# Kernel optimization log

Hardware: AMD Instinct MI355X
Metric: run time of the kernel (lower is better)

Reference implementation:

```python
import jax, jax.numpy as jnp
import numpy as np

N_NODES = 100000
N_EDGES = 1600000
D_IN = 128
D_OUT = 128
NEG_SLOPE = 0.01  # torch F.leaky_relu default


def setup_inputs() -> dict:
    key = jax.random.key(0)
    k1, k2, k3, k4, k5 = jax.random.split(key, 5)
    h = jax.random.normal(k1, (N_NODES, D_IN), dtype=jnp.float32)
    # nn.Linear default init scale ~ 1/sqrt(fan_in)
    W = jax.random.normal(k2, (D_IN, D_OUT), dtype=jnp.float32) / np.sqrt(D_IN)
    attn_w = jax.random.normal(k3, (2 * D_OUT,), dtype=jnp.float32) / np.sqrt(2 * D_OUT)
    edge_src = jax.random.randint(k4, (N_EDGES,), 0, N_NODES, dtype=jnp.int32)
    edge_dst = jax.random.randint(k5, (N_EDGES,), 0, N_NODES, dtype=jnp.int32)
    return {"h": h, "W": W, "attn_w": attn_w, "edge_src": edge_src, "edge_dst": edge_dst}


def reference(h, W, attn_w, edge_src, edge_dst):
    n = h.shape[0]
    d = W.shape[1]
    z = h @ W                                   # [N, d]
    # attention_func(cat([z_src, z_dst])) == z_src @ a[:d] + z_dst @ a[d:]
    s_src = z @ attn_w[:d]                      # [N]
    s_dst = z @ attn_w[d:]                      # [N]
    e = jax.nn.leaky_relu(s_src[edge_src] + s_dst[edge_dst], NEG_SLOPE)  # [E]
    # segment softmax over incoming edges of each dst node
    m = jax.ops.segment_max(e, edge_dst, num_segments=n)   # [N], -inf for empty
    ex = jnp.exp(e - m[edge_dst])                           # [E]
    denom = jax.ops.segment_sum(ex, edge_dst, num_segments=n)  # [N]
    alpha = ex / denom[edge_dst]                             # [E]
    # weighted neighbor sum: sum_j alpha_ij * z_j
    out = jax.ops.segment_sum(alpha[:, None] * z[edge_src], edge_dst, num_segments=n)
    return out
```

## Files before the change

kernel.cpp:

```cpp
#include <hip/hip_runtime.h>

#define D 128
#define NEG_SLOPE 0.01f
#define BSHIFT 7
#define B1 1024
#define STR 136
#define SCHUNK 3072
#define SEPT 6
#define SLOT 2560

typedef __attribute__((ext_vector_type(8))) short short8;
typedef __attribute__((ext_vector_type(4))) float floatx4;

__device__ __forceinline__ unsigned f2bf_rne(float x) {
    unsigned u = __float_as_uint(x);
    return (u + 0x7fffu + ((u >> 16) & 1u)) >> 16;
}
#define BF_LO(u) __uint_as_float((u) << 16)
#define BF_HI(u) __uint_as_float((u) & 0xffff0000u)

__global__ void init_gcur(int* __restrict__ gcur) {
    const int i = threadIdx.x;
    gcur[i] = i * SLOT;
}

__global__ __launch_bounds__(512) void sort_scatter(const int* __restrict__ esrc,
                                                    const int* __restrict__ edst,
                                                    int* __restrict__ gcur,
                                                    int* __restrict__ pairs, int E) {
    __shared__ int cnt[B1], exc[B1], gbs[B1], cur[B1];
    __shared__ int spk[SCHUNK];
    __shared__ unsigned short sbkt[SCHUNK];
    __shared__ int wtot[8];
    const int t = threadIdx.x;
    cnt[t] = 0; cnt[t + 512] = 0; cur[t] = 0; cur[t + 512] = 0;
    __syncthreads();

    const int e0 = blockIdx.x * SCHUNK;
    const int n  = min(SCHUNK, E - e0);

    int pk[SEPT], bk[SEPT];
#pragma unroll
    for (int k = 0; k < SEPT; ++k) {
        const int i = t + k * 512;
        if (i < n) {
            const int d = edst[e0 + i];
            const int s = esrc[e0 + i];
            bk[k] = d >> BSHIFT;
            pk[k] = (s << BSHIFT) | (d & 127);
            atomicAdd(&cnt[bk[k]], 1);
        } else {
            bk[k] = -1;
        }
    }
    __syncthreads();

    const int c0 = cnt[2 * t], c1 = cnt[2 * t + 1];
    const int s2 = c0 + c1;
    int incl = s2;
#pragma unroll
    for (int o = 1; o < 64; o <<= 1) {
        int v = __shfl_up(incl, o, 64);
        if ((t & 63) >= o) incl += v;
    }
    const int wv = t >> 6;
    if ((t & 63) == 63) wtot[wv] = incl;
    __syncthreads();
    int wpre = 0;
#pragma unroll
    for (int i = 0; i < 8; ++i) wpre += (i < wv) ? wtot[i] : 0;
    const int ex0 = wpre + incl - s2;
    exc[2 * t]     = ex0;
    exc[2 * t + 1] = ex0 + c0;
    if (c0 > 0) gbs[2 * t]     = atomicAdd(&gcur[2 * t], c0);
    if (c1 > 0) gbs[2 * t + 1] = atomicAdd(&gcur[2 * t + 1], c1);
    __syncthreads();

#pragma unroll
    for (int k = 0; k < SEPT; ++k) {
        if (bk[k] >= 0) {
            const int p = exc[bk[k]] + atomicAdd(&cur[bk[k]], 1);
            spk[p]  = pk[k];
            sbkt[p] = (unsigned short)bk[k];
        }
    }
    __syncthreads();

    for (int i = t; i < n; i += 512) {
        const int b = sbkt[i];
        const int pos = gbs[b] + (i - exc[b]);
        if (pos < (b + 1) * SLOT) pairs[pos] = spk[i];
    }
}

__global__ __launch_bounds__(256) void fine_build(const int* __restrict__ pairs,
                                                  const int* __restrict__ gcur,
                                                  int* __restrict__ beg,
                                                  int* __restrict__ ncnt,
                                                  int* __restrict__ adj, int N) {
    __shared__ int cnt[128], sc[128], cur[128];
    const int b = blockIdx.x;
    const int base = b << BSHIFT;
    const int nd = min(128, N - base);
    const int t = threadIdx.x;
    const int s0 = b * SLOT;
    const int e1 = min(gcur[b], s0 + SLOT);
    if (t < 128) { cnt[t] = 0; cur[t] = 0; }
    __syncthreads();
    int pk[10];
#pragma unroll
    for (int k = 0; k < 10; ++k) {
        const int i = s0 + t + k * 256;
        pk[k] = (i < e1) ? pairs[i] : -1;
        if (pk[k] >= 0) atomicAdd(&cnt[pk[k] & 127], 1);
    }
    __syncthreads();
    if (t < 128) sc[t] = cnt[t];
    __syncthreads();
    for (int off = 1; off < 128; off <<= 1) {
        int v = (t < 128 && t >= off) ? sc[t - off] : 0;
        __syncthreads();
        if (t < 128) sc[t] += v;
        __syncthreads();
    }
    if (t < nd) {
        beg[base + t]  = s0 + sc[t] - cnt[t];
        ncnt[base + t] = cnt[t];
    }
    __syncthreads();
#pragma unroll
    for (int k = 0; k < 10; ++k) {
        if (pk[k] >= 0) {
            const int d = pk[k] & 127;
            const int pos = s0 + (sc[d] - cnt[d]) + atomicAdd(&cur[d], 1);
            adj[pos] = pk[k] >> BSHIFT;
        }
    }
}

__global__ __launch_bounds__(256) void gemm_zs(const float* __restrict__ h,
                                               const float* __restrict__ W,
                                               const float* __restrict__ aw,
                                               unsigned short* __restrict__ z,
                                               float* __restrict__ s_src,
                                               float* __restrict__ s_dst, int N) {
    __shared__ unsigned short ws_hi[D * STR];
    __shared__ unsigned short ws_lo[D * STR];
    const int t = threadIdx.x;
    for (int i = t; i < D * D; i += 256) {
        int k = i >> 7, n = i & 127;
        float x = W[i];
        unsigned hi = f2bf_rne(x);
        float hf = __uint_as_float(hi << 16);
        unsigned lo = __float_as_uint(x - hf) >> 16;
        ws_hi[n * STR + k] = (unsigned short)hi;
        ws_lo[n * STR + k] = (unsigned short)lo;
    }
    __syncthreads();

    const int lane = t & 63, quad = lane >> 4, l16 = lane & 15;
    const int rowbase = blockIdx.x * 64 + (t >> 6) * 16;
    const int arow = min(rowbase + l16, N - 1);
    const float* __restrict__ hrow = h + (size_t)arow * D;

    floatx4 acc[8];
#pragma unroll
    for (int ct = 0; ct < 8; ++ct) acc[ct] = (floatx4){0.f, 0.f, 0.f, 0.f};

#pragma unroll
    for (int kk = 0; kk < 4; ++kk) {
        const int k0 = kk * 32 + quad * 8;
        float4 x0 = *(const float4*)&hrow[k0];
        float4 x1 = *(const float4*)&hrow[k0 + 4];
        float xs[8] = {x0.x, x0.y, x0.z, x0.w, x1.x, x1.y, x1.z, x1.w};
        union { short8 v; unsigned short u[8]; } ahi, alo;
#pragma unroll
        for (int i = 0; i < 8; ++i) {
            unsigned hi = f2bf_rne(xs[i]);
            float hf = __uint_as_float(hi << 16);
            ahi.u[i] = (unsigned short)hi;
            alo.u[i] = (unsigned short)(__float_as_uint(xs[i] - hf) >> 16);
        }
#pragma unroll
        for (int ct = 0; ct < 8; ++ct) {
            const int bo = (ct * 16 + l16) * STR + k0;
            short8 bhi = *(const short8*)&ws_hi[bo];
            short8 blo = *(const short8*)&ws_lo[bo];
            acc[ct] = __builtin_amdgcn_mfma_f32_16x16x32_bf16(ahi.v, bhi, acc[ct], 0, 0, 0);
            acc[ct] = __builtin_amdgcn_mfma_f32_16x16x32_bf16(alo.v, bhi, acc[ct], 0, 0, 0);
            acc[ct] = __builtin_amdgcn_mfma_f32_16x16x32_bf16(ahi.v, blo, acc[ct], 0, 0, 0);
        }
    }

#pragma unroll
    for (int ct = 0; ct < 8; ++ct)
#pragma unroll
        for (int reg = 0; reg < 4; ++reg) {
            int r = rowbase + quad * 4 + reg;
            if (r < N)
                z[(size_t)r * D + ct * 16 + l16] = (unsigned short)f2bf_rne(acc[ct][reg]);
        }

    float ps[4] = {0.f, 0.f, 0.f, 0.f}, pd[4] = {0.f, 0.f, 0.f, 0.f};
#pragma unroll
    for (int ct = 0; ct < 8; ++ct) {
        float as = aw[ct * 16 + l16];
        float ad = aw[128 + ct * 16 + l16];
#pragma unroll
        for (int reg = 0; reg < 4; ++reg) {
            ps[reg] = fmaf(acc[ct][reg], as, ps[reg]);
            pd[reg] = fmaf(acc[ct][reg], ad, pd[reg]);
        }
    }
#pragma unroll
    for (int reg = 0; reg < 4; ++reg)
#pragma unroll
        for (int o = 1; o < 16; o <<= 1) {
            ps[reg] += __shfl_xor(ps[reg], o, 64);
            pd[reg] += __shfl_xor(pd[reg], o, 64);
        }
    if (l16 == 0) {
#pragma unroll
        for (int reg = 0; reg < 4; ++reg) {
            int r = rowbase + quad * 4 + reg;
            if (r < N) { s_src[r] = ps[reg]; s_dst[r] = pd[reg]; }
        }
    }
}

__global__ __launch_bounds__(256) void aggregate(const unsigned short* __restrict__ z,
                                                 const float* __restrict__ s_src,
                                                 const float* __restrict__ s_dst,
                                                 const int* __restrict__ beg_,
                                                 const int* __restrict__ ncnt_,
                                                 const int* __restrict__ adj,
                                                 float* __restrict__ out, int N) {
    const int lane = threadIdx.x & 63;
    const int half = lane >> 5;
    const int l32  = lane & 31;
    const int q2   = l32 >> 4;
    const int l16  = lane & 15;
    const int hb   = half << 5;
    const int pairBase = blockIdx.x * 8 + (threadIdx.x >> 6) * 2;
    if (pairBase >= N) return;
    const int nodeA = pairBase, nodeB = pairBase + 1;
    const int cA = ncnt_[nodeA], bA = beg_[nodeA];
    int cB = 0, bB = 0;
    if (nodeB < N) { cB = ncnt_[nodeB]; bB = beg_[nodeB]; }

    auto fma8 = [&](float* ac, float w, const uint4& v) {
        ac[0] = fmaf(w, BF_LO(v.x), ac[0]); ac[1] = fmaf(w, BF_HI(v.x), ac[1]);
        ac[2] = fmaf(w, BF_LO(v.y), ac[2]); ac[3] = fmaf(w, BF_HI(v.y), ac[3]);
        ac[4] = fmaf(w, BF_LO(v.z), ac[4]); ac[5] = fmaf(w, BF_HI(v.z), ac[5]);
        ac[6] = fmaf(w, BF_LO(v.w), ac[6]); ac[7] = fmaf(w, BF_HI(v.w), ac[7]);
    };

    if (max(cA, cB) <= 32) {
        const int myn = pairBase + half;
        const int mb  = half ? bB : bA;
        const int mc  = half ? cB : cA;
        const float sd = s_dst[myn < N ? myn : 0];
        int s = 0; float e = -INFINITY;
        if (l32 < mc) {
            s = adj[mb + l32];
            float tt = s_src[s] + sd;
            e = (tt >= 0.f) ? tt : NEG_SLOPE * tt;
        }
        int sj[4]; uint4 zv[4];
#pragma unroll
        for (int u = 0; u < 4; ++u) sj[u] = __shfl(s, hb + u * 2 + q2, 64);
#pragma unroll
        for (int u = 0; u < 4; ++u)
            zv[u] = *(const uint4*)&z[(size_t)sj[u] * D + l16 * 8];

        float mx = e;
#pragma unroll
        for (int o = 16; o; o >>= 1) mx = fmaxf(mx, __shfl_xor(mx, o, 64));
        float ex = (l32 < mc) ? __expf(e - mx) : 0.f;
        float sum = ex;
#pragma unroll
        for (int o = 16; o; o >>= 1) sum += __shfl_xor(sum, o, 64);
        const float inv = (mc > 0) ? 1.f / sum : 0.f;
        const float w = ex * inv;

        float a[8] = {0.f,0.f,0.f,0.f,0.f,0.f,0.f,0.f};
        float bacc[8] = {0.f,0.f,0.f,0.f,0.f,0.f,0.f,0.f};
#pragma unroll
        for (int u = 0; u < 4; ++u) {
            const int ji = u * 2 + q2;
            float wj = __shfl(w, hb + ji, 64);
            wj = (ji < mc) ? wj : 0.f;
            fma8((u & 1) ? bacc : a, wj, zv[u]);
        }
        for (int jj = 8; jj < mc; jj += 8) {
            int ji2[4]; float wj[4]; int sj2[4];
#pragma unroll
            for (int u = 0; u < 4; ++u) {
                ji2[u] = jj + u * 2 + q2;
                wj[u]  = __shfl(w, hb + ji2[u], 64);
                sj2[u] = __shfl(s, hb + ji2[u], 64);
                wj[u]  = (ji2[u] < mc) ? wj[u] : 0.f;
            }
            uint4 z0 = *(const uint4*)&z[(size_t)sj2[0] * D + l16 * 8];
            uint4 z1 = *(const uint4*)&z[(size_t)sj2[1] * D + l16 * 8];
            uint4 z2 = *(const uint4*)&z[(size_t)sj2[2] * D + l16 * 8];
            uint4 z3 = *(const uint4*)&z[(size_t)sj2[3] * D + l16 * 8];
            fma8(a, wj[0], z0);
            fma8(bacc, wj[1], z1);
            fma8(a, wj[2], z2);
            fma8(bacc, wj[3], z3);
        }
#pragma unroll
        for (int i = 0; i < 8; ++i) {
            a[i] += bacc[i];
            a[i] += __shfl_xor(a[i], 16, 64);
        }
        if (q2 == 0 && myn < N) {
            float* o = &out[(size_t)myn * D + l16 * 8];
            *(float4*)o       = make_float4(a[0], a[1], a[2], a[3]);
            *(float4*)(o + 4) = make_float4(a[4], a[5], a[6], a[7]);
        }
        return;
    }

    const int q = lane >> 4;
    for (int which = 0; which < 2; ++which) {
        const int myn = which ? nodeB : nodeA;
        if (myn >= N) break;
        const int mb = which ? bB : bA;
        const int mc = which ? cB : cA;
        const float sd = s_dst[myn];
        float a[8] = {0.f,0.f,0.f,0.f,0.f,0.f,0.f,0.f};
        float bacc[8] = {0.f,0.f,0.f,0.f,0.f,0.f,0.f,0.f};
        float mx = -INFINITY;
        for (int j = lane; j < mc; j += 64) {
            float tt = s_src[adj[mb + j]] + sd;
            tt = (tt >= 0.f) ? tt : NEG_SLOPE * tt;
            mx = fmaxf(mx, tt);
        }
#pragma unroll
        for (int o = 32; o; o >>= 1) mx = fmaxf(mx, __shfl_xor(mx, o, 64));
        float sum = 0.f;
        for (int j = lane; j < mc; j += 64) {
            float tt = s_src[adj[mb + j]] + sd;
            tt = (tt >= 0.f) ? tt : NEG_SLOPE * tt;
            sum += __expf(tt - mx);
        }
#pragma unroll
        for (int o = 32; o; o >>= 1) sum += __shfl_xor(sum, o, 64);
        const float inv = (mc > 0) ? 1.f / sum : 0.f;
        for (int base2 = 0; base2 < mc; base2 += 64) {
            const int cc = min(64, mc - base2);
            int s = 0; float w = 0.f;
            if (lane < cc) {
                s = adj[mb + base2 + lane];
                float tt = s_src[s] + sd;
                tt = (tt >= 0.f) ? tt : NEG_SLOPE * tt;
                w = __expf(tt - mx) * inv;
            }
            for (int jj = 0; jj < cc; jj += 8) {
                const int ja = jj + q;
                const int jb = ja + 4;
                float wa = __shfl(w, ja, 64); int sa = __shfl(s, ja, 64);
                float wb = __shfl(w, jb, 64); int sb = __shfl(s, jb, 64);
                wa = (ja < cc) ? wa : 0.f;
                wb = (jb < cc) ? wb : 0.f;
                uint4 za = *(const uint4*)&z[(size_t)sa * D + l16 * 8];
                uint4 zb = *(const uint4*)&z[(size_t)sb * D + l16 * 8];
                fma8(a, wa, za);
                fma8(bacc, wb, zb);
            }
        }
#pragma unroll
        for (int i = 0; i < 8; ++i) {
            a[i] += bacc[i];
            a[i] += __shfl_xor(a[i], 16, 64);
            a[i] += __shfl_xor(a[i], 32, 64);
        }
        if (q == 0) {
            float* o = &out[(size_t)myn * D + l16 * 8];
            *(float4*)o       = make_float4(a[0], a[1], a[2], a[3]);
            *(float4*)(o + 4) = make_float4(a[4], a[5], a[6], a[7]);
        }
    }
}

extern "C" void kernel_launch(void* const* d_in, const int* in_sizes, int n_in,
                              void* d_out, int out_size, void* d_ws, size_t ws_size,
                              hipStream_t stream) {
    const float* h    = (const float*)d_in[0];
    const float* W    = (const float*)d_in[1];
    const float* aw   = (const float*)d_in[2];
    const int*   esrc = (const int*)d_in[3];
    const int*   edst = (const int*)d_in[4];
    float* out = (float*)d_out;

    const int N = in_sizes[0] / D;
    const int E = in_sizes[3];
    const int NB1   = (N + 127) >> BSHIFT;
    const int NSORT = (E + SCHUNK - 1) / SCHUNK;

    char* p = (char*)d_ws;
    auto carve = [&](size_t bytes) {
        void* r = (void*)p;
        p += (bytes + 255) & ~size_t(255);
        return r;
    };
    unsigned short* z = (unsigned short*)carve(size_t(N) * D * sizeof(unsigned short));
    float* s_src  = (float*)carve(size_t(N) * sizeof(float));
    float* s_dst  = (float*)carve(size_t(N) * sizeof(float));
    int*   pairs  = (int*)carve(size_t(NB1) * SLOT * sizeof(int));
    int*   adj    = (int*)carve(size_t(NB1) * SLOT * sizeof(int));
    int*   beg    = (int*)carve(size_t(N) * sizeof(int));
    int*   ncnt   = (int*)carve(size_t(N) * sizeof(int));
    int*   gcur   = (int*)carve(size_t(B1) * sizeof(int));
    (void)ws_size; (void)n_in; (void)out_size;

    init_gcur<<<1, B1, 0, stream>>>(gcur);
    sort_scatter<<<NSORT, 512, 0, stream>>>(esrc, edst, gcur, pairs, E);
    fine_build<<<NB1, 256, 0, stream>>>(pairs, gcur, beg, ncnt, adj, N);
    gemm_zs<<<(N + 63) / 64, 256, 0, stream>>>(h, W, aw, z, s_src, s_dst, N);
    aggregate<<<(N + 7) / 8, 256, 0, stream>>>(z, s_src, s_dst, beg, ncnt, adj, out, N);
}
```

Measured before the change: 241.3 us.

## Use 1024-thread sort blocks, loop fine_build over pairs, make GEMM persistent

The sort_scatter kernel now runs 1024 threads per block over 4096-edge chunks. Its two-per-thread warp-shuffle scan is replaced by a simple shared-memory Hillis-Steele scan over 1024 buckets. fine_build now re-reads pairs from global memory in strided loops instead of holding a fixed 10-register array. gemm_zs becomes a persistent grid-stride kernel capped at 521 blocks, so the W bf16 split into shared memory happens fewer times. The trade-off is a scan with many barriers and fewer GEMM blocks to hide latency.

```diff
diff --git a/kernel.cpp b/kernel.cpp
--- a/kernel.cpp
+++ b/kernel.cpp
@@ -5,8 +5,7 @@
 #define BSHIFT 7
 #define B1 1024
 #define STR 136
-#define SCHUNK 3072
-#define SEPT 6
+#define SCHUNK 4096
 #define SLOT 2560
 
 typedef __attribute__((ext_vector_type(8))) short short8;
@@ -24,25 +23,24 @@
     gcur[i] = i * SLOT;
 }
 
-__global__ __launch_bounds__(512) void sort_scatter(const int* __restrict__ esrc,
-                                                    const int* __restrict__ edst,
-                                                    int* __restrict__ gcur,
-                                                    int* __restrict__ pairs, int E) {
+__global__ __launch_bounds__(1024) void sort_scatter(const int* __restrict__ esrc,
+                                                     const int* __restrict__ edst,
+                                                     int* __restrict__ gcur,
+                                                     int* __restrict__ pairs, int E) {
     __shared__ int cnt[B1], exc[B1], gbs[B1], cur[B1];
     __shared__ int spk[SCHUNK];
     __shared__ unsigned short sbkt[SCHUNK];
-    __shared__ int wtot[8];
     const int t = threadIdx.x;
-    cnt[t] = 0; cnt[t + 512] = 0; cur[t] = 0; cur[t + 512] = 0;
+    cnt[t] = 0; cur[t] = 0;
     __syncthreads();
 
     const int e0 = blockIdx.x * SCHUNK;
     const int n  = min(SCHUNK, E - e0);
 
-    int pk[SEPT], bk[SEPT];
-#pragma unroll
-    for (int k = 0; k < SEPT; ++k) {
-        const int i = t + k * 512;
+    int pk[4], bk[4];
+#pragma unroll
+    for (int k = 0; k < 4; ++k) {
+        const int i = t + k * 1024;
         if (i < n) {
             const int d = edst[e0 + i];
             const int s = esrc[e0 + i];
@@ -55,29 +53,21 @@
     }
     __syncthreads();
 
-    const int c0 = cnt[2 * t], c1 = cnt[2 * t + 1];
-    const int s2 = c0 + c1;
-    int incl = s2;
-#pragma unroll
-    for (int o = 1; o < 64; o <<= 1) {
-        int v = __shfl_up(incl, o, 64);
-        if ((t & 63) >= o) incl += v;
-    }
-    const int wv = t >> 6;
-    if ((t & 63) == 63) wtot[wv] = incl;
-    __syncthreads();
-    int wpre = 0;
-#pragma unroll
-    for (int i = 0; i < 8; ++i) wpre += (i < wv) ? wtot[i] : 0;
-    const int ex0 = wpre + incl - s2;
-    exc[2 * t]     = ex0;
-    exc[2 * t + 1] = ex0 + c0;
-    if (c0 > 0) gbs[2 * t]     = atomicAdd(&gcur[2 * t], c0);
-    if (c1 > 0) gbs[2 * t + 1] = atomicAdd(&gcur[2 * t + 1], c1);
-    __syncthreads();
-
-#pragma unroll
-    for (int k = 0; k < SEPT; ++k) {
+    exc[t] = cnt[t];
+    __syncthreads();
+    for (int off = 1; off < B1; off <<= 1) {
+        int v = (t >= off) ? exc[t - off] : 0;
+        __syncthreads();
+        exc[t] += v;
+        __syncthreads();
+    }
+    const int myexc = exc[t] - cnt[t];
+    exc[t] = myexc;
+    if (cnt[t] > 0) gbs[t] = atomicAdd(&gcur[t], cnt[t]);
+    __syncthreads();
+
+#pragma unroll
+    for (int k = 0; k < 4; ++k) {
         if (bk[k] >= 0) {
             const int p = exc[bk[k]] + atomicAdd(&cur[bk[k]], 1);
             spk[p]  = pk[k];
@@ -86,7 +76,7 @@
     }
     __syncthreads();
 
-    for (int i = t; i < n; i += 512) {
+    for (int i = t; i < n; i += 1024) {
         const int b = sbkt[i];
         const int pos = gbs[b] + (i - exc[b]);
         if (pos < (b + 1) * SLOT) pairs[pos] = spk[i];
@@ -107,13 +97,8 @@
     const int e1 = min(gcur[b], s0 + SLOT);
     if (t < 128) { cnt[t] = 0; cur[t] = 0; }
     __syncthreads();
-    int pk[10];
-#pragma unroll
-    for (int k = 0; k < 10; ++k) {
-        const int i = s0 + t + k * 256;
-        pk[k] = (i < e1) ? pairs[i] : -1;
-        if (pk[k] >= 0) atomicAdd(&cnt[pk[k] & 127], 1);
-    }
+    for (int i = s0 + t; i < e1; i += 256)
+        atomicAdd(&cnt[pairs[i] & 127], 1);
     __syncthreads();
     if (t < 128) sc[t] = cnt[t];
     __syncthreads();
@@ -128,13 +113,11 @@
         ncnt[base + t] = cnt[t];
     }
     __syncthreads();
-#pragma unroll
-    for (int k = 0; k < 10; ++k) {
-        if (pk[k] >= 0) {
-            const int d = pk[k] & 127;
-            const int pos = s0 + (sc[d] - cnt[d]) + atomicAdd(&cur[d], 1);
-            adj[pos] = pk[k] >> BSHIFT;
-        }
+    for (int i = s0 + t; i < e1; i += 256) {
+        const int pkv = pairs[i];
+        const int d = pkv & 127;
+        const int pos = s0 + (sc[d] - cnt[d]) + atomicAdd(&cur[d], 1);
+        adj[pos] = pkv >> BSHIFT;
     }
 }
 
@@ -143,7 +126,8 @@
                                                const float* __restrict__ aw,
                                                unsigned short* __restrict__ z,
                                                float* __restrict__ s_src,
-                                               float* __restrict__ s_dst, int N) {
+                                               float* __restrict__ s_dst,
+                                               int N, int ntiles) {
     __shared__ unsigned short ws_hi[D * STR];
     __shared__ unsigned short ws_lo[D * STR];
     const int t = threadIdx.x;
@@ -159,71 +143,74 @@
     __syncthreads();
 
     const int lane = t & 63, quad = lane >> 4, l16 = lane & 15;
-    const int rowbase = blockIdx.x * 64 + (t >> 6) * 16;
-    const int arow = min(rowbase + l16, N - 1);
-    const float* __restrict__ hrow = h + (size_t)arow * D;
-
-    floatx4 acc[8];
-#pragma unroll
-    for (int ct = 0; ct < 8; ++ct) acc[ct] = (floatx4){0.f, 0.f, 0.f, 0.f};
-
-#pragma unroll
-    for (int kk = 0; kk < 4; ++kk) {
-        const int k0 = kk * 32 + quad * 8;
-        float4 x0 = *(const float4*)&hrow[k0];
-        float4 x1 = *(const float4*)&hrow[k0 + 4];
-        float xs[8] = {x0.x, x0.y, x0.z, x0.w, x1.x, x1.y, x1.z, x1.w};
-        union { short8 v; unsigned short u[8]; } ahi, alo;
-#pragma unroll
-        for (int i = 0; i < 8; ++i) {
-            unsigned hi = f2bf_rne(xs[i]);
-            float hf = __uint_as_float(hi << 16);
-            ahi.u[i] = (unsigned short)hi;
-            alo.u[i] = (unsigned short)(__float_as_uint(xs[i] - hf) >> 16);
-        }
+
+    for (int tile = blockIdx.x; tile < ntiles; tile += gridDim.x) {
+        const int rowbase = tile * 64 + (t >> 6) * 16;
+        const int arow = min(rowbase + l16, N - 1);
+        const float* __restrict__ hrow = h + (size_t)arow * D;
+
+        floatx4 acc[8];
+#pragma unroll
+        for (int ct = 0; ct < 8; ++ct) acc[ct] = (floatx4){0.f, 0.f, 0.f, 0.f};
+
+#pragma unroll
+        for (int kk = 0; kk < 4; ++kk) {
+            const int k0 = kk * 32 + quad * 8;
+            float4 x0 = *(const float4*)&hrow[k0];
+            float4 x1 = *(const float4*)&hrow[k0 + 4];
+            float xs[8] = {x0.x, x0.y, x0.z, x0.w, x1.x, x1.y, x1.z, x1.w};
+            union { short8 v; unsigned short u[8]; } ahi, alo;
+#pragma unroll
+            for (int i = 0; i < 8; ++i) {
+                unsigned hi = f2bf_rne(xs[i]);
+                float hf = __uint_as_float(hi << 16);
+                ahi.u[i] = (unsigned short)hi;
+                alo.u[i] = (unsigned short)(__float_as_uint(xs[i] - hf) >> 16);
+            }
+#pragma unroll
+            for (int ct = 0; ct < 8; ++ct) {
+                const int bo = (ct * 16 + l16) * STR + k0;
+                short8 bhi = *(const short8*)&ws_hi[bo];
+                short8 blo = *(const short8*)&ws_lo[bo];
+                acc[ct] = __builtin_amdgcn_mfma_f32_16x16x32_bf16(ahi.v, bhi, acc[ct], 0, 0, 0);
+                acc[ct] = __builtin_amdgcn_mfma_f32_16x16x32_bf16(alo.v, bhi, acc[ct], 0, 0, 0);
+                acc[ct] = __builtin_amdgcn_mfma_f32_16x16x32_bf16(ahi.v, blo, acc[ct], 0, 0, 0);
+            }
+        }
+
+#pragma unroll
+        for (int ct = 0; ct < 8; ++ct)
+#pragma unroll
+            for (int reg = 0; reg < 4; ++reg) {
+                int r = rowbase + quad * 4 + reg;
+                if (r < N)
+                    z[(size_t)r * D + ct * 16 + l16] = (unsigned short)f2bf_rne(acc[ct][reg]);
+            }
+
+        float ps[4] = {0.f, 0.f, 0.f, 0.f}, pd[4] = {0.f, 0.f, 0.f, 0.f};
 #pragma unroll
         for (int ct = 0; ct < 8; ++ct) {
-            const int bo = (ct * 16 + l16) * STR + k0;
-            short8 bhi = *(const short8*)&ws_hi[bo];
-            short8 blo = *(const short8*)&ws_lo[bo];
-            acc[ct] = __builtin_amdgcn_mfma_f32_16x16x32_bf16(ahi.v, bhi, acc[ct], 0, 0, 0);
-            acc[ct] = __builtin_amdgcn_mfma_f32_16x16x32_bf16(alo.v, bhi, acc[ct], 0, 0, 0);
-            acc[ct] = __builtin_amdgcn_mfma_f32_16x16x32_bf16(ahi.v, blo, acc[ct], 0, 0, 0);
-        }
-    }
-
-#pragma unroll
-    for (int ct = 0; ct < 8; ++ct)
-#pragma unroll
-        for (int reg = 0; reg < 4; ++reg) {
-            int r = rowbase + quad * 4 + reg;
-            if (r < N)
-                z[(size_t)r * D + ct * 16 + l16] = (unsigned short)f2bf_rne(acc[ct][reg]);
-        }
-
-    float ps[4] = {0.f, 0.f, 0.f, 0.f}, pd[4] = {0.f, 0.f, 0.f, 0.f};
-#pragma unroll
-    for (int ct = 0; ct < 8; ++ct) {
-        float as = aw[ct * 16 + l16];
-        float ad = aw[128 + ct * 16 + l16];
-#pragma unroll
-        for (int reg = 0; reg < 4; ++reg) {
-            ps[reg] = fmaf(acc[ct][reg], as, ps[reg]);
-            pd[reg] = fmaf(acc[ct][reg], ad, pd[reg]);
-        }
-    }
-#pragma unroll
-    for (int reg = 0; reg < 4; ++reg)
-#pragma unroll
-        for (int o = 1; o < 16; o <<= 1) {
-            ps[reg] += __shfl_xor(ps[reg], o, 64);
-            pd[reg] += __shfl_xor(pd[reg], o, 64);
-        }
-    if (l16 == 0) {
-#pragma unroll
-        for (int reg = 0; reg < 4; ++reg) {
-            int r = rowbase + quad * 4 + reg;
-            if (r < N) { s_src[r] = ps[reg]; s_dst[r] = pd[reg]; }
+            float as = aw[ct * 16 + l16];
+            float ad = aw[128 + ct * 16 + l16];
+#pragma unroll
+            for (int reg = 0; reg < 4; ++reg) {
+                ps[reg] = fmaf(acc[ct][reg], as, ps[reg]);
+                pd[reg] = fmaf(acc[ct][reg], ad, pd[reg]);
+            }
+        }
+#pragma unroll
+        for (int reg = 0; reg < 4; ++reg)
+#pragma unroll
+            for (int o = 1; o < 16; o <<= 1) {
+                ps[reg] += __shfl_xor(ps[reg], o, 64);
+                pd[reg] += __shfl_xor(pd[reg], o, 64);
+            }
+        if (l16 == 0) {
+#pragma unroll
+            for (int reg = 0; reg < 4; ++reg) {
+                int r = rowbase + quad * 4 + reg;
+                if (r < N) { s_src[r] = ps[reg]; s_dst[r] = pd[reg]; }
+            }
         }
     }
 }
@@ -397,8 +384,10 @@
 
     const int N = in_sizes[0] / D;
     const int E = in_sizes[3];
-    const int NB1   = (N + 127) >> BSHIFT;
-    const int NSORT = (E + SCHUNK - 1) / SCHUNK;
+    const int NB1    = (N + 127) >> BSHIFT;
+    const int NSORT  = (E + SCHUNK - 1) / SCHUNK;
+    const int NTILES = (N + 63) / 64;
+    const int NGEMM  = min(NTILES, 521);
 
     char* p = (char*)d_ws;
     auto carve = [&](size_t bytes) {
@@ -417,8 +406,8 @@
     (void)ws_size; (void)n_in; (void)out_size;
 
     init_gcur<<<1, B1, 0, stream>>>(gcur);
-    sort_scatter<<<NSORT, 512, 0, stream>>>(esrc, edst, gcur, pairs, E);
+    sort_scatter<<<NSORT, 1024, 0, stream>>>(esrc, edst, gcur, pairs, E);
     fine_build<<<NB1, 256, 0, stream>>>(pairs, gcur, beg, ncnt, adj, N);
-    gemm_zs<<<(N + 63) / 64, 256, 0, stream>>>(h, W, aw, z, s_src, s_dst, N);
+    gemm_zs<<<NGEMM, 256, 0, stream>>>(h, W, aw, z, s_src, s_dst, N, NTILES);
     aggregate<<<(N + 7) / 8, 256, 0, stream>>>(z, s_src, s_dst, beg, ncnt, adj, out, N);
 }
```

After: 247.3 us. 1.02x slower.
